# Optimization experiments

Measured on AMD Instinct MI355X. Metric: run time of the kernel, lower is better.

## Reference

```python
import jax, jax.numpy as jnp
import numpy as np

N = 4096          # samples
D_FEAT = 256      # embedding dim
N_CLASSES = 64
N_NEIGHBORS = 3


def _sq_dists(x):
    # torch.cdist(x, x, p=2).pow(2): squared euclidean pairwise distances
    x2 = jnp.sum(x * x, axis=1)
    d = x2[:, None] + x2[None, :] - 2.0 * (x @ x.T)
    return jnp.maximum(d, 0.0)


def setup_inputs() -> dict:
    key = jax.random.key(0)
    k1, k2 = jax.random.split(key)
    outputs = jax.random.normal(k1, (N, D_FEAT), dtype=jnp.float32)
    label_inds = jax.random.randint(k2, (N,), 0, N_CLASSES)
    return {"outputs": outputs, "label_inds": label_inds, "n_neighbors": N_NEIGHBORS}


def reference(outputs, label_inds, n_neighbors):
    n = outputs.shape[0]
    D = _sq_dists(outputs)                                    # [n, n]

    # _select_targets: per-class k-NN == masked global k-NN (same squared dists)
    same = label_inds[:, None] == label_inds[None, :]
    eye = jnp.eye(n, dtype=bool)
    dd = jnp.where(same & ~eye, D, jnp.inf)
    _, tn = jax.lax.top_k(-dd, n_neighbors)                   # [n, k] target neighbors (global idx)

    target_d = jnp.take_along_axis(D, tn, axis=1)             # [n, k]
    pull = jnp.sum(target_d)
    margin_radii = 1.0 + jnp.max(target_d, axis=1)            # [n]

    # mask: True everywhere except target neighbors and the diagonal
    rows = jnp.arange(n)[:, None]
    mask = jnp.ones((n, n), dtype=bool).at[rows, tn].set(False) & ~eye

    # Original broadcast (max_dist [n,1] vs distance [n,1,n]) yields
    #   push = sum_i sum_{a,j} relu(margin_radii[i] - D[a,j]) * mask[a,j]
    # i.e. each r_i is compared against ALL masked distances. Compute this
    # O(n^3)-element sum exactly in O(n^2 log n) via sort + prefix sums:
    #   sum_d relu(r - d) = r * #{d < r} - sum_{d < r} d
    d_flat = jnp.where(mask.reshape(-1), D.reshape(-1), jnp.inf)
    d_sorted = jnp.sort(d_flat)
    csum = jnp.cumsum(jnp.where(jnp.isinf(d_sorted), 0.0, d_sorted))
    csum0 = jnp.concatenate([jnp.zeros((1,), D.dtype), csum])
    counts = jnp.searchsorted(d_sorted, margin_radii, side='left')  # strict d < r
    push = jnp.sum(margin_radii * counts.astype(D.dtype) - csum0[counts])

    return (pull + push) / n
```

## Files before the change

kernel.cpp:

```cpp
#include <hip/hip_runtime.h>
#include <hip/hip_bf16.h>
#include <float.h>

#define N 4096
#define DF 256
#define NB2 2048
#define MAXM 128
#define NPUSHBLK 528

typedef __attribute__((ext_vector_type(8))) short short8v;
typedef __attribute__((ext_vector_type(8))) unsigned short ushort8v;
typedef __attribute__((ext_vector_type(4))) float floatx4;

__device__ inline unsigned short f2bf(float f) {
    __hip_bfloat16 h = __float2bfloat16(f);
    return *reinterpret_cast<unsigned short*>(&h);
}
__device__ inline float bf2f(unsigned short h) {
    unsigned int u = ((unsigned int)h) << 16;
    return __uint_as_float(u);
}

__device__ inline void gload_lds16(const void* g, void* l) {
    __builtin_amdgcn_global_load_lds((const __attribute__((address_space(1))) void*)g,
                                     (__attribute__((address_space(3))) void*)l, 16, 0, 0);
}

__global__ __launch_bounds__(256) void prep_kernel(const float* __restrict__ X,
                                                   const int* __restrict__ labels,
                                                   float* __restrict__ x2,
                                                   __hip_bfloat16* __restrict__ Xb,
                                                   int* __restrict__ cnt,
                                                   int* __restrict__ members,
                                                   double* __restrict__ accd,
                                                   unsigned int* __restrict__ tickets,
                                                   int useXb) {
    int t = threadIdx.x;
    if (blockIdx.x == 1024) {
        __shared__ int scnt[64];
        if (t < 8) accd[t] = 0.0;
        if (t == 8) { tickets[0] = 0u; tickets[1] = 0u; }
        if (t < 64) scnt[t] = 0;
        __syncthreads();
        for (int i = t; i < N; i += 256) {
            int c = labels[i];
            int pos = atomicAdd(&scnt[c], 1);
            if (pos < MAXM) members[(c << 8) + pos] = i;
        }
        __syncthreads();
        if (t < 64) cnt[t] = min(scnt[t], MAXM);
        return;
    }
    int row = blockIdx.x * 4 + (t >> 6);
    int l = t & 63;
    int idx = row * 64 + l;
    float4 v = ((const float4*)X)[idx];
    if (useXb) {
        ushort4 o;
        o.x = f2bf(v.x); o.y = f2bf(v.y); o.z = f2bf(v.z); o.w = f2bf(v.w);
        ((ushort4*)Xb)[idx] = o;
    }
    float s = v.x * v.x + v.y * v.y + v.z * v.z + v.w * v.w;
#pragma unroll
    for (int off = 32; off > 0; off >>= 1) s += __shfl_xor(s, off, 64);
    if (l == 0) x2[row] = s;
}

__device__ inline void top3_upd(float& b0, float& b1, float& b2, float dd) {
    if (dd < b2) {
        if (dd < b1) { b2 = b1; if (dd < b0) { b1 = b0; b0 = dd; } else b1 = dd; }
        else b2 = dd;
    }
}

__global__ __launch_bounds__(512) void knn4_kernel(const float* __restrict__ X,
                                                   const float* __restrict__ x2,
                                                   const int* __restrict__ cnt,
                                                   const int* __restrict__ members,
                                                   float* __restrict__ ptop) {
    __shared__ __align__(16) char smem[32768];
    __shared__ int marr[MAXM];
    __shared__ float mx2[MAXM];

    int c = blockIdx.x & 63;
    int q = blockIdx.x >> 6;
    int m = cnt[c];
    if (q * 32 >= m) return;
    const int* mem = members + (c << 8);
    int tid = threadIdx.x;
    int lane = tid & 63;
    int wid = tid >> 6;
    int qbase = q * 32;

    if (tid < MAXM) {
        int mi = (tid < m) ? mem[tid] : -1;
        marr[tid] = mi;
        mx2[tid] = (mi >= 0) ? x2[mi] : 0.f;
    }
    __syncthreads();

    char* Hi = smem;
    char* Lo = smem + 16384;

#pragma unroll
    for (int it = 0; it < 2; ++it) {
        int idx = it * 512 + tid;
        int rb = idx >> 9;
        int rem = idx & 511;
        int kb = rem >> 4;
        int r0 = rem & 15;
        int rg = qbase + rb * 16 + r0;
        ushort8v vhi = (ushort8v){0,0,0,0,0,0,0,0};
        ushort8v vlo = vhi;
        if (rg < m) {
            const float4* src = (const float4*)(X + (size_t)marr[rg] * DF + kb * 8);
            float4 u0 = src[0], u1 = src[1];
            float uu[8] = {u0.x, u0.y, u0.z, u0.w, u1.x, u1.y, u1.z, u1.w};
#pragma unroll
            for (int p = 0; p < 8; ++p) {
                unsigned short h = f2bf(uu[p]);
                vhi[p] = h;
                vlo[p] = f2bf(uu[p] - bf2f(h));
            }
        }
        *((ushort8v*)(Hi + ((size_t)idx << 4))) = vhi;
        *((ushort8v*)(Lo + ((size_t)idx << 4))) = vlo;
    }
    __syncthreads();

    int nstripe = (m + 15) >> 4;
    if (wid >= nstripe) return;

    int arow = wid * 16 + (lane & 15);
    bool avalid = (arow < m);
    const float* aptr = X + (size_t)(avalid ? marr[arow] : 0) * DF;
    int ko = (lane >> 4) * 8;
    short8v aHi[8], aLo[8];
#pragma unroll
    for (int kk = 0; kk < 8; ++kk) {
        ushort8v vhi = (ushort8v){0,0,0,0,0,0,0,0};
        ushort8v vlo = vhi;
        if (avalid) {
            const float* p0 = aptr + kk * 32 + ko;
            float4 u0 = *(const float4*)p0;
            float4 u1 = *(const float4*)(p0 + 4);
            float uu[8] = {u0.x, u0.y, u0.z, u0.w, u1.x, u1.y, u1.z, u1.w};
#pragma unroll
            for (int p = 0; p < 8; ++p) {
                unsigned short h = f2bf(uu[p]);
                vhi[p] = h;
                vlo[p] = f2bf(uu[p] - bf2f(h));
            }
        }
        aHi[kk] = *(short8v*)&vhi;
        aLo[kk] = *(short8v*)&vlo;
    }

    int g = lane >> 4;
    int cl = lane & 15;
    float x2i[4];
#pragma unroll
    for (int r = 0; r < 4; ++r) {
        int il = wid * 16 + g * 4 + r;
        x2i[r] = mx2[il];
    }

    float t0[4], t1[4], t2[4];
#pragma unroll
    for (int r = 0; r < 4; ++r) { t0[r] = FLT_MAX; t1[r] = FLT_MAX; t2[r] = FLT_MAX; }

#pragma unroll
    for (int ct = 0; ct < 2; ++ct) {
        floatx4 acc = (floatx4){0.f, 0.f, 0.f, 0.f};
#pragma unroll
        for (int kk = 0; kk < 8; ++kk) {
            size_t off = (size_t)ct * 8192 + (size_t)kk * 1024 + ((size_t)lane << 4);
            short8v bHi = *((const short8v*)(Hi + off));
            short8v bLo = *((const short8v*)(Lo + off));
            acc = __builtin_amdgcn_mfma_f32_16x16x32_bf16(aLo[kk], bHi, acc, 0, 0, 0);
            acc = __builtin_amdgcn_mfma_f32_16x16x32_bf16(aHi[kk], bLo, acc, 0, 0, 0);
            acc = __builtin_amdgcn_mfma_f32_16x16x32_bf16(aHi[kk], bHi, acc, 0, 0, 0);
        }
        int jg = qbase + ct * 16 + cl;
        float x2j = (jg < MAXM) ? mx2[jg] : 0.f;
#pragma unroll
        for (int r = 0; r < 4; ++r) {
            int il = wid * 16 + g * 4 + r;
            float d = fmaxf(x2i[r] + x2j - 2.f * acc[r], 0.f);
            bool valid = (jg < m) && (il < m) && (jg != il);
            top3_upd(t0[r], t1[r], t2[r], valid ? d : FLT_MAX);
        }
    }

#pragma unroll
    for (int off = 1; off <= 8; off <<= 1) {
#pragma unroll
        for (int r = 0; r < 4; ++r) {
            float c0 = __shfl_xor(t0[r], off, 64);
            float c1 = __shfl_xor(t1[r], off, 64);
            float c2 = __shfl_xor(t2[r], off, 64);
            float m0, m1, m2;
            if (t0[r] <= c0) {
                m0 = t0[r];
                if (t1[r] <= c0) { m1 = t1[r]; m2 = fminf(t2[r], c0); }
                else { m1 = c0; m2 = fminf(t1[r], c1); }
            } else {
                m0 = c0;
                if (c1 <= t0[r]) { m1 = c1; m2 = fminf(c2, t0[r]); }
                else { m1 = t0[r]; m2 = fminf(c1, t1[r]); }
            }
            t0[r] = m0; t1[r] = m1; t2[r] = m2;
        }
    }
    if (cl == 0) {
#pragma unroll
        for (int r = 0; r < 4; ++r) {
            int il = wid * 16 + g * 4 + r;
            if (il < m) {
                int gi = marr[il];
                float* dst = ptop + ((size_t)q * N + gi) * 3;
                dst[0] = t0[r]; dst[1] = t1[r]; dst[2] = t2[r];
            }
        }
    }
}

__global__ __launch_bounds__(1024) void histo_ftab_kernel(const int* __restrict__ labels,
                                                          const int* __restrict__ cnt,
                                                          const float* __restrict__ ptop,
                                                          float* __restrict__ fv_g,
                                                          float* __restrict__ hdr,
                                                          double* __restrict__ accd) {
    __shared__ int cntb[NB2];
    __shared__ float sumb[NB2];
    __shared__ float fv[NB2 + 1];
    __shared__ float aux[64];
    __shared__ int iaux[16];
    int t = threadIdx.x;
    int wid = t >> 6, lane = t & 63;

    float rad[4];
    float td[4][3];
#pragma unroll
    for (int s = 0; s < 4; ++s) {
        int i = t + s * 1024;
        int c = labels[i];
        int m = cnt[c];
        int nq = min(4, (m + 31) >> 5);
        const float* p0 = ptop + (size_t)i * 3;
        float a0 = p0[0], a1 = p0[1], a2 = p0[2];
        for (int qq = 1; qq < nq; ++qq) {
            const float* pq = ptop + ((size_t)qq * N + i) * 3;
            float b0 = pq[0], b1 = pq[1], b2 = pq[2];
            float m0, m1, m2;
            if (a0 <= b0) {
                m0 = a0;
                if (a1 <= b0) { m1 = a1; m2 = fminf(a2, b0); }
                else { m1 = b0; m2 = fminf(a1, b1); }
            } else {
                m0 = b0;
                if (b1 <= a0) { m1 = b1; m2 = fminf(b2, a0); }
                else { m1 = a0; m2 = fminf(b1, a1); }
            }
            a0 = m0; a1 = m1; a2 = m2;
        }
        td[s][0] = a0; td[s][1] = a1; td[s][2] = a2;
        rad[s] = 1.f + a2;
    }

    float mn = fminf(fminf(rad[0], rad[1]), fminf(rad[2], rad[3]));
    float mx = fmaxf(fmaxf(rad[0], rad[1]), fmaxf(rad[2], rad[3]));
#pragma unroll
    for (int off = 32; off > 0; off >>= 1) {
        mn = fminf(mn, __shfl_xor(mn, off, 64));
        mx = fmaxf(mx, __shfl_xor(mx, off, 64));
    }
    if (lane == 0) { aux[wid] = mn; aux[wid + 16] = mx; }
    cntb[t] = 0; cntb[t + 1024] = 0;
    sumb[t] = 0.f; sumb[t + 1024] = 0.f;
    __syncthreads();
    mn = aux[0]; mx = aux[16];
    for (int w = 1; w < 16; ++w) { mn = fminf(mn, aux[w]); mx = fmaxf(mx, aux[w + 16]); }
    float range = fmaxf(mx - mn, 1e-30f);
    float scale = (float)NB2 / range * (1.f - 1e-6f);

#pragma unroll
    for (int s = 0; s < 4; ++s) {
        int b = max(0, min((int)((rad[s] - mn) * scale), NB2 - 1));
        atomicAdd(&cntb[b], 1);
        atomicAdd(&sumb[b], rad[s]);
    }
    __syncthreads();

    int c0 = cntb[2 * t], c1 = cntb[2 * t + 1];
    float s0 = sumb[2 * t], s1 = sumb[2 * t + 1];
    int toti = c0 + c1;
    float totf = s0 + s1;
    int sci = toti;
    float scf = totf;
#pragma unroll
    for (int off = 1; off < 64; off <<= 1) {
        int yi = __shfl_down(sci, off, 64);
        float yf = __shfl_down(scf, off, 64);
        if (lane + off < 64) { sci += yi; scf += yf; }
    }
    if (lane == 0) { iaux[wid] = sci; aux[wid] = scf; }
    __syncthreads();
    if (t < 16) {
        int xi = iaux[t];
        float xf = aux[t];
        int si = xi;
        float sf = xf;
#pragma unroll
        for (int off = 1; off < 16; off <<= 1) {
            int yi = __shfl_down(si, off, 64);
            float yf = __shfl_down(sf, off, 64);
            if (t + off < 16) { si += yi; sf += yf; }
        }
        iaux[t] = si - xi;
        aux[t] = sf - xf;
    }
    __syncthreads();
    int afteri = iaux[wid] + (sci - toti);
    float afterf = aux[wid] + (scf - totf);
    int C1 = c1 + afteri, C0 = c0 + C1;
    float S1 = s1 + afterf, S0 = s0 + S1;

    float wbin = range / (float)NB2;
    {
        float x0 = mn + wbin * (float)(2 * t);
        fv[2 * t + 0] = S0 - x0 * (float)C0;
        float x1 = mn + wbin * (float)(2 * t + 1);
        fv[2 * t + 1] = S1 - x1 * (float)C1;
    }
    if (t == 0) fv[NB2] = 0.f;
    __syncthreads();

    for (int b = t; b <= NB2; b += 1024)
        fv_g[b] = fv[b];
    float Stot = fv[0] + mn * (float)N;
    float invw = (float)NB2 / fmaxf(mx - mn, 1e-20f);
    if (t == 0) {
        hdr[0] = mn;
        hdr[1] = mx;
        hdr[2] = invw;
        hdr[3] = Stot;
    }

    float loc = 0.f, pul = 0.f;
#pragma unroll
    for (int s = 0; s < 4; ++s) {
#pragma unroll
        for (int k = 0; k < 3; ++k) {
            float d = td[s][k];
            pul += d;
            if (d >= mx) continue;
            if (d < mn) {
                loc += fmaf(-d, (float)N, Stot);
            } else {
                float tpos = (d - mn) * invw;
                int b = min((int)tpos, NB2 - 1);
                float frac = tpos - (float)b;
                loc += fmaf(frac, fv[b + 1] - fv[b], fv[b]);
            }
        }
    }
#pragma unroll
    for (int off = 32; off > 0; off >>= 1) {
        loc += __shfl_xor(loc, off, 64);
        pul += __shfl_xor(pul, off, 64);
    }
    __syncthreads();
    if (lane == 0) { aux[wid] = loc; aux[wid + 16] = pul; }
    __syncthreads();
    if (t == 0) {
        float s = 0.f, p = 0.f;
        for (int w = 0; w < 16; ++w) { s += aux[w]; p += aux[w + 16]; }
        accd[2] = (double)s;
        accd[0] = (double)p;
    }
}

template<int USEXB>
__global__ __launch_bounds__(256) void push_gemm_kernel(const float* __restrict__ X,
                                                        const __hip_bfloat16* __restrict__ Xb,
                                                        const float* __restrict__ x2,
                                                        const float* __restrict__ fv_g,
                                                        const float* __restrict__ hdr,
                                                        float* __restrict__ pp,
                                                        unsigned int* __restrict__ tickets,
                                                        const double* __restrict__ accd,
                                                        float* __restrict__ out) {
    __shared__ __align__(16) char smem[32768];
    __shared__ __align__(16) float fvP[NB2 + 1];
    __shared__ float x2r[128], x2c[128];
    __shared__ float red[256];
    __shared__ double wsumD[4];
    __shared__ int lastFlag;

    int bid = blockIdx.x;
    int by = 0, rem = bid;
    while (rem >= 32 - by) { rem -= 32 - by; ++by; }
    int bx = by + rem;
    int rowBase = by * 128, colBase = bx * 128;

    int tid = threadIdx.x;
    int lane = tid & 63;
    int wv = tid >> 6;
    int wy = wv >> 1, wx = wv & 1;

    floatx4 acc4[4][4];
#pragma unroll
    for (int m = 0; m < 4; ++m)
#pragma unroll
        for (int n = 0; n < 4; ++n) acc4[m][n] = (floatx4){0.f, 0.f, 0.f, 0.f};

    if (tid < 128) { x2r[tid] = x2[rowBase + tid]; x2c[tid] = x2[colBase + tid]; }
    for (int i = tid; i <= NB2; i += 256) fvP[i] = fv_g[i];

    for (int k0 = 0; k0 < DF; k0 += 64) {
        if (k0) __syncthreads();
        if (USEXB) {
            const __hip_bfloat16* Ab = Xb + (size_t)rowBase * DF;
            const __hip_bfloat16* Bb = Xb + (size_t)colBase * DF;
#pragma unroll
            for (int i = 0; i < 4; ++i) {
                int did = wv * 256 + i * 64 + lane;
                int row = ((did >> 7) << 4) | (did & 15);
                int kb = (did >> 4) & 7;
                size_t goff = (size_t)row * DF + k0 + kb * 8;
                char* ldsA = smem + (size_t)(wv * 256 + i * 64) * 16;
                gload_lds16(Ab + goff, ldsA);
                gload_lds16(Bb + goff, ldsA + 16384);
            }
        } else {
#pragma unroll
            for (int cch = 0; cch < 4; ++cch) {
                int did = tid + (cch << 8);
                int row = ((did >> 7) << 4) | (did & 15);
                int kb = (did >> 4) & 7;
                const float* srcA = X + (size_t)(rowBase + row) * DF + k0 + kb * 8;
                const float* srcB = X + (size_t)(colBase + row) * DF + k0 + kb * 8;
                float4 a0 = *(const float4*)srcA;
                float4 a1 = *(const float4*)(srcA + 4);
                float4 e0 = *(const float4*)srcB;
                float4 e1 = *(const float4*)(srcB + 4);
                ushort8v va, vb;
                va[0] = f2bf(a0.x); va[1] = f2bf(a0.y); va[2] = f2bf(a0.z); va[3] = f2bf(a0.w);
                va[4] = f2bf(a1.x); va[5] = f2bf(a1.y); va[6] = f2bf(a1.z); va[7] = f2bf(a1.w);
                vb[0] = f2bf(e0.x); vb[1] = f2bf(e0.y); vb[2] = f2bf(e0.z); vb[3] = f2bf(e0.w);
                vb[4] = f2bf(e1.x); vb[5] = f2bf(e1.y); vb[6] = f2bf(e1.z); vb[7] = f2bf(e1.w);
                *((ushort8v*)(smem + (did << 4))) = va;
                *((ushort8v*)(smem + 16384 + (did << 4))) = vb;
            }
        }
        __syncthreads();
#pragma unroll
        for (int kk = 0; kk < 2; ++kk) {
            short8v a[4], b[4];
#pragma unroll
            for (int m = 0; m < 4; ++m)
                a[m] = *((const short8v*)(smem + (((wy * 4 + m) * 2 + kk) << 10) + (lane << 4)));
#pragma unroll
            for (int n = 0; n < 4; ++n)
                b[n] = *((const short8v*)(smem + 16384 + (((wx * 4 + n) * 2 + kk) << 10) + (lane << 4)));
#pragma unroll
            for (int m = 0; m < 4; ++m)
#pragma unroll
                for (int n = 0; n < 4; ++n)
                    acc4[m][n] = __builtin_amdgcn_mfma_f32_16x16x32_bf16(a[m], b[n], acc4[m][n], 0, 0, 0);
        }
    }
    __syncthreads();

    float d0v = hdr[0], rmaxv = hdr[1], invw = hdr[2], Stot = hdr[3];
    bool diag = (by == bx);

    float local = 0.f;
    int g = lane >> 4;
    int cl = lane & 15;
#pragma unroll
    for (int m = 0; m < 4; ++m) {
#pragma unroll
        for (int n = 0; n < 4; ++n) {
            floatx4 v = acc4[m][n];
            int gcl = wx * 64 + n * 16 + cl;
            float x2cv = x2c[gcl];
#pragma unroll
            for (int r = 0; r < 4; ++r) {
                int grl = wy * 64 + m * 16 + g * 4 + r;
                if (diag && grl == gcl) continue;
                float d = fmaxf(x2r[grl] + x2cv - 2.f * v[r], 0.f);
                if (d >= rmaxv) continue;
                if (d < d0v) {
                    local += fmaf(-d, (float)N, Stot);
                } else {
                    float tpos = (d - d0v) * invw;
                    int b = min((int)tpos, NB2 - 1);
                    float frac = tpos - (float)b;
                    float fa = fvP[b];
                    float fb = fvP[b + 1];
                    local += fmaf(frac, fb - fa, fa);
                }
            }
        }
    }
    red[tid] = local;
    __syncthreads();
    for (int s2 = 128; s2 > 0; s2 >>= 1) {
        if (tid < s2) red[tid] += red[tid + s2];
        __syncthreads();
    }
    if (tid == 0) {
        float wt = diag ? 1.f : 2.f;
        pp[bid] = wt * red[0];
        __threadfence();
        unsigned int old = atomicAdd(&tickets[1], 1u);
        lastFlag = (old == NPUSHBLK - 1) ? 1 : 0;
    }
    __syncthreads();

    if (lastFlag) {
        __threadfence();
        double s = 0.0;
        for (int i = tid; i < NPUSHBLK; i += 256) s += (double)pp[i];
#pragma unroll
        for (int off = 32; off > 0; off >>= 1) s += __shfl_down(s, off, 64);
        if (lane == 0) wsumD[wv] = s;
        __syncthreads();
        if (tid == 0) {
            double tot = wsumD[0] + wsumD[1] + wsumD[2] + wsumD[3];
            out[0] = (float)((accd[0] + tot - accd[2]) / (double)N);
        }
    }
}

extern "C" void kernel_launch(void* const* d_in, const int* in_sizes, int n_in,
                              void* d_out, int out_size, void* d_ws, size_t ws_size,
                              hipStream_t stream) {
    const float* X = (const float*)d_in[0];
    const int* labels = (const int*)d_in[1];
    float* out = (float*)d_out;

    char* w = (char*)d_ws;
    double* accd   = (double*)w;
    float* x2      = (float*)(w + 64);
    float* ptop    = (float*)(w + 16448);
    int* cnt       = (int*)(w + 213056);
    int* members   = (int*)(w + 213312);
    float* hdr     = (float*)(w + 278848);
    float* fv_g    = (float*)(w + 278912);
    float* pp      = (float*)(w + 287168);
    unsigned int* tickets = (unsigned int*)(w + 289280);
    __hip_bfloat16* Xb = (__hip_bfloat16*)(w + 289344);
    size_t need_xb = 289344 + (size_t)N * DF * 2;
    int useXb = (ws_size >= need_xb) ? 1 : 0;

    hipLaunchKernelGGL(prep_kernel, dim3(1025), dim3(256), 0, stream,
                       X, labels, x2, Xb, cnt, members, accd, tickets, useXb);
    hipLaunchKernelGGL(knn4_kernel, dim3(256), dim3(512), 0, stream,
                       X, x2, cnt, members, ptop);
    hipLaunchKernelGGL(histo_ftab_kernel, dim3(1), dim3(1024), 0, stream,
                       labels, cnt, ptop, fv_g, hdr, accd);
    if (useXb)
        hipLaunchKernelGGL(push_gemm_kernel<1>, dim3(NPUSHBLK), dim3(256), 0, stream,
                           X, Xb, x2, fv_g, hdr, pp, tickets, accd, out);
    else
        hipLaunchKernelGGL(push_gemm_kernel<0>, dim3(NPUSHBLK), dim3(256), 0, stream,
                           X, Xb, x2, fv_g, hdr, pp, tickets, accd, out);
}
```

Before: 66.14 us.

## Fold histogram/ftab stage into push GEMM kernel via leader block and flag

Removes the single-block histo_ftab kernel launch. The first block to grab a ticket in push_gemm now builds the radius histogram, prefix table and pull/local sums, then publishes a global flag. All other blocks run their GEMM tiles at the same time and spin on that flag only before the epilogue that needs the table. This hides the serial histogram work behind the GEMM and saves a launch, but the leader block does extra work, and the spin-wait assumes the leader block is scheduled.

```diff
diff --git a/kernel.cpp b/kernel.cpp
--- a/kernel.cpp
+++ b/kernel.cpp
@@ -24,6 +24,20 @@
 __device__ inline void gload_lds16(const void* g, void* l) {
     __builtin_amdgcn_global_load_lds((const __attribute__((address_space(1))) void*)g,
                                      (__attribute__((address_space(3))) void*)l, 16, 0, 0);
+}
+
+__device__ inline void merge3(float& a0, float& a1, float& a2, float b0, float b1, float b2) {
+    float m0, m1, m2;
+    if (a0 <= b0) {
+        m0 = a0;
+        if (a1 <= b0) { m1 = a1; m2 = fminf(a2, b0); }
+        else { m1 = b0; m2 = fminf(a1, b1); }
+    } else {
+        m0 = b0;
+        if (b1 <= a0) { m1 = b1; m2 = fminf(b2, a0); }
+        else { m1 = a0; m2 = fminf(b1, a1); }
+    }
+    a0 = m0; a1 = m1; a2 = m2;
 }
 
 __global__ __launch_bounds__(256) void prep_kernel(const float* __restrict__ X,
@@ -39,7 +53,7 @@
     if (blockIdx.x == 1024) {
         __shared__ int scnt[64];
         if (t < 8) accd[t] = 0.0;
-        if (t == 8) { tickets[0] = 0u; tickets[1] = 0u; }
+        if (t < 16) tickets[t] = 0u;
         if (t < 64) scnt[t] = 0;
         __syncthreads();
         for (int i = t; i < N; i += 256) {
@@ -225,171 +239,18 @@
     }
 }
 
-__global__ __launch_bounds__(1024) void histo_ftab_kernel(const int* __restrict__ labels,
-                                                          const int* __restrict__ cnt,
-                                                          const float* __restrict__ ptop,
-                                                          float* __restrict__ fv_g,
-                                                          float* __restrict__ hdr,
-                                                          double* __restrict__ accd) {
-    __shared__ int cntb[NB2];
-    __shared__ float sumb[NB2];
-    __shared__ float fv[NB2 + 1];
-    __shared__ float aux[64];
-    __shared__ int iaux[16];
-    int t = threadIdx.x;
-    int wid = t >> 6, lane = t & 63;
-
-    float rad[4];
-    float td[4][3];
-#pragma unroll
-    for (int s = 0; s < 4; ++s) {
-        int i = t + s * 1024;
-        int c = labels[i];
-        int m = cnt[c];
-        int nq = min(4, (m + 31) >> 5);
-        const float* p0 = ptop + (size_t)i * 3;
-        float a0 = p0[0], a1 = p0[1], a2 = p0[2];
-        for (int qq = 1; qq < nq; ++qq) {
-            const float* pq = ptop + ((size_t)qq * N + i) * 3;
-            float b0 = pq[0], b1 = pq[1], b2 = pq[2];
-            float m0, m1, m2;
-            if (a0 <= b0) {
-                m0 = a0;
-                if (a1 <= b0) { m1 = a1; m2 = fminf(a2, b0); }
-                else { m1 = b0; m2 = fminf(a1, b1); }
-            } else {
-                m0 = b0;
-                if (b1 <= a0) { m1 = b1; m2 = fminf(b2, a0); }
-                else { m1 = a0; m2 = fminf(b1, a1); }
-            }
-            a0 = m0; a1 = m1; a2 = m2;
-        }
-        td[s][0] = a0; td[s][1] = a1; td[s][2] = a2;
-        rad[s] = 1.f + a2;
-    }
-
-    float mn = fminf(fminf(rad[0], rad[1]), fminf(rad[2], rad[3]));
-    float mx = fmaxf(fmaxf(rad[0], rad[1]), fmaxf(rad[2], rad[3]));
-#pragma unroll
-    for (int off = 32; off > 0; off >>= 1) {
-        mn = fminf(mn, __shfl_xor(mn, off, 64));
-        mx = fmaxf(mx, __shfl_xor(mx, off, 64));
-    }
-    if (lane == 0) { aux[wid] = mn; aux[wid + 16] = mx; }
-    cntb[t] = 0; cntb[t + 1024] = 0;
-    sumb[t] = 0.f; sumb[t + 1024] = 0.f;
-    __syncthreads();
-    mn = aux[0]; mx = aux[16];
-    for (int w = 1; w < 16; ++w) { mn = fminf(mn, aux[w]); mx = fmaxf(mx, aux[w + 16]); }
-    float range = fmaxf(mx - mn, 1e-30f);
-    float scale = (float)NB2 / range * (1.f - 1e-6f);
-
-#pragma unroll
-    for (int s = 0; s < 4; ++s) {
-        int b = max(0, min((int)((rad[s] - mn) * scale), NB2 - 1));
-        atomicAdd(&cntb[b], 1);
-        atomicAdd(&sumb[b], rad[s]);
-    }
-    __syncthreads();
-
-    int c0 = cntb[2 * t], c1 = cntb[2 * t + 1];
-    float s0 = sumb[2 * t], s1 = sumb[2 * t + 1];
-    int toti = c0 + c1;
-    float totf = s0 + s1;
-    int sci = toti;
-    float scf = totf;
-#pragma unroll
-    for (int off = 1; off < 64; off <<= 1) {
-        int yi = __shfl_down(sci, off, 64);
-        float yf = __shfl_down(scf, off, 64);
-        if (lane + off < 64) { sci += yi; scf += yf; }
-    }
-    if (lane == 0) { iaux[wid] = sci; aux[wid] = scf; }
-    __syncthreads();
-    if (t < 16) {
-        int xi = iaux[t];
-        float xf = aux[t];
-        int si = xi;
-        float sf = xf;
-#pragma unroll
-        for (int off = 1; off < 16; off <<= 1) {
-            int yi = __shfl_down(si, off, 64);
-            float yf = __shfl_down(sf, off, 64);
-            if (t + off < 16) { si += yi; sf += yf; }
-        }
-        iaux[t] = si - xi;
-        aux[t] = sf - xf;
-    }
-    __syncthreads();
-    int afteri = iaux[wid] + (sci - toti);
-    float afterf = aux[wid] + (scf - totf);
-    int C1 = c1 + afteri, C0 = c0 + C1;
-    float S1 = s1 + afterf, S0 = s0 + S1;
-
-    float wbin = range / (float)NB2;
-    {
-        float x0 = mn + wbin * (float)(2 * t);
-        fv[2 * t + 0] = S0 - x0 * (float)C0;
-        float x1 = mn + wbin * (float)(2 * t + 1);
-        fv[2 * t + 1] = S1 - x1 * (float)C1;
-    }
-    if (t == 0) fv[NB2] = 0.f;
-    __syncthreads();
-
-    for (int b = t; b <= NB2; b += 1024)
-        fv_g[b] = fv[b];
-    float Stot = fv[0] + mn * (float)N;
-    float invw = (float)NB2 / fmaxf(mx - mn, 1e-20f);
-    if (t == 0) {
-        hdr[0] = mn;
-        hdr[1] = mx;
-        hdr[2] = invw;
-        hdr[3] = Stot;
-    }
-
-    float loc = 0.f, pul = 0.f;
-#pragma unroll
-    for (int s = 0; s < 4; ++s) {
-#pragma unroll
-        for (int k = 0; k < 3; ++k) {
-            float d = td[s][k];
-            pul += d;
-            if (d >= mx) continue;
-            if (d < mn) {
-                loc += fmaf(-d, (float)N, Stot);
-            } else {
-                float tpos = (d - mn) * invw;
-                int b = min((int)tpos, NB2 - 1);
-                float frac = tpos - (float)b;
-                loc += fmaf(frac, fv[b + 1] - fv[b], fv[b]);
-            }
-        }
-    }
-#pragma unroll
-    for (int off = 32; off > 0; off >>= 1) {
-        loc += __shfl_xor(loc, off, 64);
-        pul += __shfl_xor(pul, off, 64);
-    }
-    __syncthreads();
-    if (lane == 0) { aux[wid] = loc; aux[wid + 16] = pul; }
-    __syncthreads();
-    if (t == 0) {
-        float s = 0.f, p = 0.f;
-        for (int w = 0; w < 16; ++w) { s += aux[w]; p += aux[w + 16]; }
-        accd[2] = (double)s;
-        accd[0] = (double)p;
-    }
-}
-
 template<int USEXB>
 __global__ __launch_bounds__(256) void push_gemm_kernel(const float* __restrict__ X,
                                                         const __hip_bfloat16* __restrict__ Xb,
                                                         const float* __restrict__ x2,
-                                                        const float* __restrict__ fv_g,
-                                                        const float* __restrict__ hdr,
+                                                        const int* __restrict__ labels,
+                                                        const int* __restrict__ cnt,
+                                                        const float* __restrict__ ptop,
+                                                        float* __restrict__ fv_g,
+                                                        float* __restrict__ hdr,
                                                         float* __restrict__ pp,
                                                         unsigned int* __restrict__ tickets,
-                                                        const double* __restrict__ accd,
+                                                        double* __restrict__ accd,
                                                         float* __restrict__ out) {
     __shared__ __align__(16) char smem[32768];
     __shared__ __align__(16) float fvP[NB2 + 1];
@@ -397,6 +258,8 @@
     __shared__ float red[256];
     __shared__ double wsumD[4];
     __shared__ int lastFlag;
+    __shared__ int bFlag;
+    __shared__ int ibx[4];
 
     int bid = blockIdx.x;
     int by = 0, rem = bid;
@@ -409,14 +272,153 @@
     int wv = tid >> 6;
     int wy = wv >> 1, wx = wv & 1;
 
+    if (tid == 0) bFlag = (atomicAdd(&tickets[2], 1u) == 0u) ? 1 : 0;
+    if (tid < 128) { x2r[tid] = x2[rowBase + tid]; x2c[tid] = x2[colBase + tid]; }
+    __syncthreads();
+
+    if (bFlag) {
+        float* radbuf = (float*)smem;
+        int* cntb = (int*)(smem + 16384);
+        float* sumb = (float*)(smem + 24576);
+
+        float mnl = FLT_MAX, mxl = -FLT_MAX;
+        for (int s = 0; s < 16; ++s) {
+            int i = tid + s * 256;
+            int c = labels[i];
+            int m = cnt[c];
+            int nq = min(4, (m + 31) >> 5);
+            const float* p0 = ptop + (size_t)i * 3;
+            float a0 = p0[0], a1 = p0[1], a2 = p0[2];
+            for (int qq = 1; qq < nq; ++qq) {
+                const float* pq = ptop + ((size_t)qq * N + i) * 3;
+                merge3(a0, a1, a2, pq[0], pq[1], pq[2]);
+            }
+            float r = 1.f + a2;
+            radbuf[i] = r;
+            mnl = fminf(mnl, r);
+            mxl = fmaxf(mxl, r);
+        }
+        {
+            int4 zz = {0, 0, 0, 0};
+            int4* z4 = (int4*)(smem + 16384);
+            z4[tid] = zz; z4[tid + 256] = zz; z4[tid + 512] = zz; z4[tid + 768] = zz;
+        }
+#pragma unroll
+        for (int off = 32; off > 0; off >>= 1) {
+            mnl = fminf(mnl, __shfl_xor(mnl, off, 64));
+            mxl = fmaxf(mxl, __shfl_xor(mxl, off, 64));
+        }
+        if (lane == 0) { red[wv] = mnl; red[8 + wv] = mxl; }
+        __syncthreads();
+        float mn = fminf(fminf(red[0], red[1]), fminf(red[2], red[3]));
+        float mx = fmaxf(fmaxf(red[8], red[9]), fmaxf(red[10], red[11]));
+        float range = fmaxf(mx - mn, 1e-30f);
+        float scale = (float)NB2 / range * (1.f - 1e-6f);
+        float wbin = range / (float)NB2;
+
+        for (int s = 0; s < 16; ++s) {
+            float v = radbuf[tid + s * 256];
+            int b = max(0, min((int)((v - mn) * scale), NB2 - 1));
+            atomicAdd(&cntb[b], 1);
+            atomicAdd(&sumb[b], v);
+        }
+        __syncthreads();
+
+        int ci[8]; float si[8];
+        int Ct = 0; float St = 0.f;
+        int base = tid * 8;
+#pragma unroll
+        for (int k = 0; k < 8; ++k) {
+            ci[k] = cntb[base + k]; si[k] = sumb[base + k];
+            Ct += ci[k]; St += si[k];
+        }
+        int sci = Ct; float scf = St;
+#pragma unroll
+        for (int off = 1; off < 64; off <<= 1) {
+            int yi = __shfl_down(sci, off, 64);
+            float yf = __shfl_down(scf, off, 64);
+            if (lane + off < 64) { sci += yi; scf += yf; }
+        }
+        __syncthreads();
+        if (lane == 0) { ibx[wv] = sci; red[wv] = scf; }
+        __syncthreads();
+        int aC = 0; float aS = 0.f;
+        for (int w2 = wv + 1; w2 < 4; ++w2) { aC += ibx[w2]; aS += red[w2]; }
+        int runC = aC + (sci - Ct);
+        float runS = aS + (scf - St);
+#pragma unroll
+        for (int k = 7; k >= 0; --k) {
+            runC += ci[k]; runS += si[k];
+            float xe = mn + wbin * (float)(base + k);
+            float f = runS - xe * (float)runC;
+            fvP[base + k] = f;
+            fv_g[base + k] = f;
+        }
+        if (tid == 0) { fvP[NB2] = 0.f; fv_g[NB2] = 0.f; }
+        __syncthreads();
+
+        float Stot = fvP[0] + mn * (float)N;
+        float invw = (float)NB2 / fmaxf(mx - mn, 1e-20f);
+
+        float loc = 0.f, pul = 0.f;
+        for (int s = 0; s < 16; ++s) {
+            int i = tid + s * 256;
+            int c = labels[i];
+            int m = cnt[c];
+            int nq = min(4, (m + 31) >> 5);
+            const float* p0 = ptop + (size_t)i * 3;
+            float a0 = p0[0], a1 = p0[1], a2 = p0[2];
+            for (int qq = 1; qq < nq; ++qq) {
+                const float* pq = ptop + ((size_t)qq * N + i) * 3;
+                merge3(a0, a1, a2, pq[0], pq[1], pq[2]);
+            }
+            float tdv[3] = {a0, a1, a2};
+#pragma unroll
+            for (int k = 0; k < 3; ++k) {
+                float d = tdv[k];
+                pul += d;
+                if (d >= mx) continue;
+                if (d < mn) {
+                    loc += fmaf(-d, (float)N, Stot);
+                } else {
+                    float tpos = (d - mn) * invw;
+                    int b = min((int)tpos, NB2 - 1);
+                    float frac = tpos - (float)b;
+                    loc += fmaf(frac, fvP[b + 1] - fvP[b], fvP[b]);
+                }
+            }
+        }
+#pragma unroll
+        for (int off = 32; off > 0; off >>= 1) {
+            loc += __shfl_xor(loc, off, 64);
+            pul += __shfl_xor(pul, off, 64);
+        }
+        __syncthreads();
+        if (lane == 0) { red[wv] = loc; red[8 + wv] = pul; }
+        __syncthreads();
+        if (tid == 0) {
+            float s = red[0] + red[1] + red[2] + red[3];
+            float p = red[8] + red[9] + red[10] + red[11];
+            accd[2] = (double)s;
+            accd[0] = (double)p;
+            hdr[0] = mn;
+            hdr[1] = mx;
+            hdr[2] = invw;
+            hdr[3] = Stot;
+        }
+        __syncthreads();
+        if (tid == 0) {
+            __threadfence();
+            atomicExch(&tickets[3], 1u);
+        }
+        __syncthreads();
+    }
+
     floatx4 acc4[4][4];
 #pragma unroll
     for (int m = 0; m < 4; ++m)
 #pragma unroll
         for (int n = 0; n < 4; ++n) acc4[m][n] = (floatx4){0.f, 0.f, 0.f, 0.f};
-
-    if (tid < 128) { x2r[tid] = x2[rowBase + tid]; x2c[tid] = x2[colBase + tid]; }
-    for (int i = tid; i <= NB2; i += 256) fvP[i] = fv_g[i];
 
     for (int k0 = 0; k0 < DF; k0 += 64) {
         if (k0) __syncthreads();
@@ -473,6 +475,15 @@
     }
     __syncthreads();
 
+    if (tid == 0) {
+        while (atomicOr(&tickets[3], 0u) == 0u) {
+            __builtin_amdgcn_s_sleep(8);
+        }
+    }
+    __syncthreads();
+    for (int i = tid; i <= NB2; i += 256) fvP[i] = fv_g[i];
+    __syncthreads();
+
     float d0v = hdr[0], rmaxv = hdr[1], invw = hdr[2], Stot = hdr[3];
     bool diag = (by == bx);
 
@@ -560,12 +571,10 @@
                        X, labels, x2, Xb, cnt, members, accd, tickets, useXb);
     hipLaunchKernelGGL(knn4_kernel, dim3(256), dim3(512), 0, stream,
                        X, x2, cnt, members, ptop);
-    hipLaunchKernelGGL(histo_ftab_kernel, dim3(1), dim3(1024), 0, stream,
-                       labels, cnt, ptop, fv_g, hdr, accd);
     if (useXb)
         hipLaunchKernelGGL(push_gemm_kernel<1>, dim3(NPUSHBLK), dim3(256), 0, stream,
-                           X, Xb, x2, fv_g, hdr, pp, tickets, accd, out);
+                           X, Xb, x2, labels, cnt, ptop, fv_g, hdr, pp, tickets, accd, out);
     else
         hipLaunchKernelGGL(push_gemm_kernel<0>, dim3(NPUSHBLK), dim3(256), 0, stream,
-                           X, Xb, x2, fv_g, hdr, pp, tickets, accd, out);
-}
+                           X, Xb, x2, labels, cnt, ptop, fv_g, hdr, pp, tickets, accd, out);
+}
```

Measured after the change: 95.53 us. +44.4%, slower.
